# Performance work log

Measured on AMD Instinct MI355X. Metric: run time of the kernel, lower is better.

Reference implementation:

```python
import jax, jax.numpy as jnp
import numpy as np
from jax import lax

B, N, C, H, W = 2, 32, 64, 128, 128
ROI_H = ROI_W = 28
RATIO = 2  # ROIAlign sampling_ratio


def setup_inputs() -> dict:
    key = jax.random.key(0)
    ks = jax.random.split(key, 20)
    p = lambda k, s: jax.random.normal(k, s, jnp.float32) * 0.05
    inp = {}
    inp['cnn_feature'] = jax.random.normal(ks[0], (B, C, H, W), jnp.float32)
    inp['act_ind'] = jax.random.randint(ks[1], (B, N), 0, H * W)
    inp['awh'] = jax.random.uniform(ks[2], (B, N, 2), jnp.float32, minval=4.0, maxval=40.0)
    # fusion: 4 convs (64->256, then 256->256 x3), all 3x3 pad 1
    inp['w1'] = p(ks[3], (256, 64, 3, 3)); inp['b1'] = jnp.zeros((256,), jnp.float32)
    inp['w2'] = p(ks[4], (256, 256, 3, 3)); inp['b2'] = jnp.zeros((256,), jnp.float32)
    inp['w3'] = p(ks[5], (256, 256, 3, 3)); inp['b3'] = jnp.zeros((256,), jnp.float32)
    inp['w4'] = p(ks[6], (256, 256, 3, 3)); inp['b4'] = jnp.zeros((256,), jnp.float32)
    # cp_hm head: deconv(256->256,k2,s2) + conv1x1(256->1), bias -2.19
    inp['hm_dw'] = p(ks[7], (256, 256, 2, 2))  # torch ConvTranspose layout [in,out,kh,kw]
    inp['hm_db'] = jnp.zeros((256,), jnp.float32)
    inp['hm_w'] = p(ks[8], (1, 256, 1, 1)); inp['hm_b'] = jnp.full((1,), -2.19, jnp.float32)
    # cp_wh head: deconv(256->256,k2,s2) + conv1x1(256->2), bias 0
    inp['wh_dw'] = p(ks[9], (256, 256, 2, 2))
    inp['wh_db'] = jnp.zeros((256,), jnp.float32)
    inp['wh_w'] = p(ks[10], (2, 256, 1, 1)); inp['wh_b'] = jnp.zeros((2,), jnp.float32)
    return inp


def conv(x, w, b, pad):
    y = lax.conv_general_dilated(x, w, (1, 1), pad, dimension_numbers=('NCHW', 'OIHW', 'NCHW'))
    return y + b[None, :, None, None]


def deconv2x2s2(x, w, b):
    # matches torch ConvTranspose2d(k=2, s=2, pad=0) with weight [in,out,2,2]
    y = lax.conv_transpose(x, w, (2, 2), 'VALID', dimension_numbers=('NCHW', 'IOHW', 'NCHW'), transpose_kernel=True)
    return y + b[None, :, None, None]


def roi_align(feat, b_idx, boxes):
    # feat [B,C,H,W], boxes [R,4] (x1,y1,x2,y2), spatial_scale=1, sampling_ratio=RATIO
    x1, y1, x2, y2 = boxes[:, 0], boxes[:, 1], boxes[:, 2], boxes[:, 3]
    bw = (x2 - x1) / ROI_W
    bh = (y2 - y1) / ROI_H
    sx = jnp.arange(ROI_W * RATIO)
    sy = jnp.arange(ROI_H * RATIO)
    # sample coord for bin i, sub-sample k: start + (i + (k+0.5)/ratio) * bin
    fx = (sx // RATIO).astype(jnp.float32) + ((sx % RATIO).astype(jnp.float32) + 0.5) / RATIO
    fy = (sy // RATIO).astype(jnp.float32) + ((sy % RATIO).astype(jnp.float32) + 0.5) / RATIO
    xs = x1[:, None] + fx[None, :] * bw[:, None]   # [R,Sx]
    ys = y1[:, None] + fy[None, :] * bh[:, None]   # [R,Sy]

    def sample_one(bi, ysr, xsr):
        img = feat[bi]                              # [C,H,W]
        ysr = jnp.clip(ysr, 0.0, H - 1.0)
        xsr = jnp.clip(xsr, 0.0, W - 1.0)
        y0 = jnp.floor(ysr).astype(jnp.int32); y1i = jnp.minimum(y0 + 1, H - 1); wy = ysr - y0
        x0 = jnp.floor(xsr).astype(jnp.int32); x1i = jnp.minimum(x0 + 1, W - 1); wx = xsr - x0
        # separable bilinear: interpolate rows, then columns
        rows = img[:, y0, :] * (1.0 - wy)[None, :, None] + img[:, y1i, :] * wy[None, :, None]  # [C,Sy,W]
        vals = rows[:, :, x0] * (1.0 - wx)[None, None, :] + rows[:, :, x1i] * wx[None, None, :]  # [C,Sy,Sx]
        # average RATIO x RATIO samples per bin
        v = vals.reshape(C, ROI_H, RATIO, ROI_W, RATIO)
        return v.mean(axis=(2, 4))                  # [C,ROI_H,ROI_W]

    return jax.vmap(sample_one)(b_idx, ys, xs)      # [R,C,ROI_H,ROI_W]


def reference(cnn_feature, act_ind, awh, w1, b1, w2, b2, w3, b3, w4, b4,
              hm_dw, hm_db, hm_w, hm_b, wh_dw, wh_db, wh_w, wh_b):
    # --- prepare_training: decode boxes from act_ind + awh (act_01 all ones) ---
    xs = (act_ind % W).astype(jnp.float32)          # [B,N]
    ys = (act_ind // W).astype(jnp.float32)
    half_w = awh[..., 0] / 2.0
    half_h = awh[..., 1] / 2.0
    boxes = jnp.stack([xs - half_w, ys - half_h, xs + half_w, ys + half_h], axis=-1)  # [B,N,4]
    boxes = boxes.reshape(B * N, 4)
    b_idx = jnp.repeat(jnp.arange(B), N)
    roi = roi_align(cnn_feature, b_idx, boxes)      # [R,64,28,28]
    # --- fusion convs ---
    x = jax.nn.relu(conv(roi, w1, b1, 'SAME'))
    x = jax.nn.relu(conv(x, w2, b2, 'SAME'))
    x = jax.nn.relu(conv(x, w3, b3, 'SAME'))
    x = jax.nn.relu(conv(x, w4, b4, 'SAME'))        # [R,256,28,28]
    # --- heads ---
    cp_hm = conv(deconv2x2s2(x, hm_dw, hm_db), hm_w, hm_b, 'VALID')  # [R,1,56,56]
    cp_wh = conv(deconv2x2s2(x, wh_dw, wh_db), wh_w, wh_b, 'VALID')  # [R,2,56,56]
    return jnp.concatenate([cp_hm, cp_wh], axis=1)  # [R,3,56,56]
```

## Files before the change

kernel.cpp:

```cpp
#include <hip/hip_runtime.h>
#include <hip/hip_bf16.h>

#define HWF 128
#define NB  64
#define PW  30
#define PP  900

using bf16 = __hip_bfloat16;
typedef __attribute__((ext_vector_type(8)))  short short8;
typedef __attribute__((ext_vector_type(4)))  float f32x4;
typedef __attribute__((ext_vector_type(16))) float f32x16;
typedef __attribute__((ext_vector_type(4)))  unsigned int u32x4;
typedef __attribute__((ext_vector_type(2)))  unsigned int u32x2;

__device__ __forceinline__ float b2f(bf16 v) { return __bfloat162float(v); }
__device__ __forceinline__ bf16  f2b(float v){ return __float2bfloat16(v); }
__device__ __forceinline__ float u2f(unsigned short u){ unsigned x = (unsigned)u << 16; float f; __builtin_memcpy(&f,&x,4); return f; }
__device__ __forceinline__ unsigned pack2(float a, float b) {
  union { bf16 h; unsigned short u; } ca, cb; ca.h = f2b(a); cb.h = f2b(b);
  return ((unsigned)cb.u << 16) | (unsigned)ca.u;
}

__global__ void weff_kernel(const float* __restrict__ hm_dw, const float* __restrict__ hm_db,
                            const float* __restrict__ hm_w,  const float* __restrict__ hm_b,
                            const float* __restrict__ wh_dw, const float* __restrict__ wh_db,
                            const float* __restrict__ wh_w,  const float* __restrict__ wh_b,
                            float* __restrict__ Weff, float* __restrict__ beff) {
  const int blk = blockIdx.x;
  const int k = blk / 3, o = blk % 3;
  const int ci = threadIdx.x;
  const float* dw = (o == 0) ? hm_dw : wh_dw;
  const float* hw = (o == 0) ? hm_w  : (wh_w + (size_t)(o - 1) * 256);
  const float* dwp = dw + (size_t)ci * 4 + k;
  float s = 0.f;
  for (int co = 0; co < 256; ++co) s += hw[co] * dwp[(size_t)co * 1024];
  Weff[(size_t)blk * 256 + ci] = s;
  if (k == 0 && ci == 0) {
    const float* db = (o == 0) ? hm_db : wh_db;
    float bb = (o == 0) ? hm_b[0] : wh_b[o - 1];
    float t = 0.f;
    for (int co = 0; co < 256; ++co) t += hw[co] * db[co];
    beff[o] = bb + t;
  }
}

__global__ void wt_kernel(const float* __restrict__ w, bf16* __restrict__ Wt, int CIN) {
  const int co = blockIdx.x, ci = threadIdx.x;
  const int NCIB = CIN >> 5;
  const int cib = ci >> 5, cl = ci & 31;
  const int kh = cl >> 4, koct = (cl >> 3) & 1, e = ci & 7;
  for (int tap = 0; tap < 9; ++tap)
    Wt[(((((size_t)tap * NCIB + cib) * 2 + kh) * 256 + co) * 2 + koct) * 8 + e]
        = f2b(w[((size_t)co * CIN + ci) * 9 + tap]);
}

__global__ __launch_bounds__(256) void featT_kernel(const float* __restrict__ feat,
                                                    bf16* __restrict__ featT) {
  const int by = blockIdx.x;
  const int b = by >> 7, y = by & 127;
  const int t = threadIdx.x;
  __shared__ float tile[128][65];
  const int xr = t & 127, c2 = t >> 7;
  for (int c0 = 0; c0 < 64; c0 += 2)
    tile[xr][c0 + c2] = feat[(((size_t)(b * 64 + c0 + c2) * 128 + y) * 128) + xr];
  __syncthreads();
  const int cw = t & 63, x4 = t >> 6;
  for (int x0 = 0; x0 < 128; x0 += 4)
    featT[(((size_t)by * 128) + x0 + x4) * 64 + cw] = f2b(tile[x0 + x4][cw]);
}

__global__ __launch_bounds__(256) void roi_cl(const bf16* __restrict__ featT,
                                              const int* __restrict__ act_ind,
                                              const float* __restrict__ awh,
                                              bf16* __restrict__ roiP) {
  const int r = blockIdx.x, part = blockIdx.y;
  const int t = threadIdx.x;
  if (part == 7) {
    for (int i = t; i < 116 * 64; i += 256) {
      int j = i >> 6, c = i & 63;
      int py, px;
      if (j < 30)      { py = 0;      px = j;      }
      else if (j < 60) { py = 29;     px = j - 30; }
      else if (j < 88) { py = j - 59; px = 0;      }
      else             { py = j - 87; px = 29;     }
      roiP[(((size_t)(r * 2 + (c >> 5)) * PP) + py * PW + px) * 32 + (c & 31)] = f2b(0.f);
    }
    return;
  }
  const int wave = t >> 6, c = t & 63;
  const int bi = r >> 5;
  const int ind = act_ind[r];
  const float cx = (float)(ind % HWF), cy = (float)(ind / HWF);
  const float hw = awh[r * 2 + 0] * 0.5f, hh = awh[r * 2 + 1] * 0.5f;
  const float x1b = cx - hw, y1b = cy - hh;
  const float bw = hw / 14.f, bh = hh / 14.f;
  const bf16* fb = featT + (size_t)bi * HWF * HWF * 64;
  for (int pp = part * 112 + wave; pp < part * 112 + 112; pp += 4) {
    int ry = pp / 28, rx = pp % 28;
    float acc = 0.f;
#pragma unroll
    for (int a = 0; a < 2; ++a) {
      int syi = 2 * ry + a;
      float ys = y1b + ((float)syi * 0.5f + 0.25f) * bh;
      ys = fminf(fmaxf(ys, 0.f), 127.f);
      int y0 = (int)floorf(ys); int y1i = min(y0 + 1, 127);
      float wy = ys - (float)y0;
#pragma unroll
      for (int b2 = 0; b2 < 2; ++b2) {
        int sxi = 2 * rx + b2;
        float xs = x1b + ((float)sxi * 0.5f + 0.25f) * bw;
        xs = fminf(fmaxf(xs, 0.f), 127.f);
        int x0 = (int)floorf(xs); int x1i = min(x0 + 1, 127);
        float wx = xs - (float)x0;
        float v00 = b2f(fb[((size_t)y0  * HWF + x0 ) * 64 + c]);
        float v01 = b2f(fb[((size_t)y0  * HWF + x1i) * 64 + c]);
        float v10 = b2f(fb[((size_t)y1i * HWF + x0 ) * 64 + c]);
        float v11 = b2f(fb[((size_t)y1i * HWF + x1i) * 64 + c]);
        float r0 = v00 * (1.f - wy) + v10 * wy;
        float r1 = v01 * (1.f - wy) + v11 * wy;
        acc += r0 * (1.f - wx) + r1 * wx;
      }
    }
    int slot = (ry + 1) * PW + (rx + 1);
    roiP[(((size_t)(r * 2 + (c >> 5)) * PP) + slot) * 32 + (c & 31)] = f2b(acc * 0.25f);
  }
}

template <int CIN>
__global__ __launch_bounds__(256, 2) void conv_mfma(const bf16* __restrict__ X,
                                                    const bf16* __restrict__ Wt,
                                                    const float* __restrict__ bias,
                                                    bf16* __restrict__ Y) {
  constexpr int NCIB = CIN / 32;
  const int d = blockIdx.x;
  const int xcd = d & 7, sub = d >> 3;
  const int img = xcd * 8 + (sub >> 4);
  const int sm  = sub & 15;
  const int sb  = sm >> 2;
  const int mg  = sm & 3;
  const int s0  = 30 + sb * 210;
  const int gbase = s0 - 31;
  const int t = threadIdx.x;
  const int wave = t >> 6, lane = t & 63;
  const int hi = lane >> 5, l31 = lane & 31;
  const int ng = wave;

  __shared__ char lds_raw[71680];
  char* Ab = lds_raw;
  char* Bb = lds_raw + 36864;

  int bsrc[5]; bool bok[5];
#pragma unroll
  for (int r = 0; r < 5; ++r) {
    int chunk = r * 256 + t;
    bok[r] = (chunk < 1088);
    int ss = chunk >> 2, up = chunk & 3;
    int u = up ^ ((ss >> 2) & 3);
    int q = gbase + ss; q = q < 0 ? 0 : (q > 899 ? 899 : q);
    bsrc[r] = q * 64 + u * 16;
  }

#define STAGE_B(BSEL, CIB)                                                       \
  {                                                                              \
    const char* Xc = (const char*)X + ((size_t)(img * NCIB + (CIB)) * 900) * 64; \
    _Pragma("unroll")                                                            \
    for (int r = 0; r < 5; ++r) {                                                \
      if (bok[r]) {                                                              \
        __builtin_amdgcn_global_load_lds(                                        \
            (const __attribute__((address_space(1))) unsigned int*)(Xc + bsrc[r]),\
            (__attribute__((address_space(3))) unsigned int*)                    \
                (Bb + (BSEL) * 17408 + r * 4096 + wave * 1024), 16, 0, 0);       \
      }                                                                          \
    }                                                                            \
  }

  const int kh_w = t >> 7;
  const int cl127 = t & 127;

#define STAGE_A(CIB)                                                             \
  {                                                                              \
    _Pragma("unroll")                                                            \
    for (int t9 = 0; t9 < 9; ++t9) {                                             \
      const char* src = (const char*)Wt +                                        \
          (((size_t)(t9 * NCIB + (CIB)) * 2 + kh_w) * 8192) + mg * 2048          \
          + cl127 * 16;                                                          \
      __builtin_amdgcn_global_load_lds(                                          \
          (const __attribute__((address_space(1))) unsigned int*)src,            \
          (__attribute__((address_space(3))) unsigned int*)                      \
              (Ab + t9 * 4096 + wave * 1024), 16, 0, 0);                         \
    }                                                                            \
  }

  f32x16 acc[2][2];
#pragma unroll
  for (int mf = 0; mf < 2; ++mf)
#pragma unroll
    for (int nf = 0; nf < 2; ++nf)
#pragma unroll
      for (int e = 0; e < 16; ++e) acc[mf][nf][e] = 0.f;

  int soc[2];
#pragma unroll
  for (int nf = 0; nf < 2; ++nf) {
    int so = ng * 64 + nf * 32 + l31;
    soc[nf] = (so > 209 ? 209 : so) + 31;
  }

  constexpr int DTP[9] = { -31, -30, -29, -1, 0, 1, 29, 30, 31 };

#define LOADA(A, J)                                                              \
  {                                                                              \
    _Pragma("unroll")                                                            \
    for (int mf = 0; mf < 2; ++mf) {                                             \
      A[mf] = *(const short8*)(Ab + ((J) >> 1) * 4096 + ((J) & 1) * 2048         \
                               + (mf * 32 + l31) * 32 + hi * 16);                \
    }                                                                            \
  }

#define LOADB(B, LB, J)                                                          \
  {                                                                              \
    _Pragma("unroll")                                                            \
    for (int nf = 0; nf < 2; ++nf) {                                             \
      int ss = soc[nf] + DTP[(J) >> 1];                                          \
      int u = ((((J) & 1) << 1) + hi) ^ ((ss >> 2) & 3);                         \
      B[nf] = *(const short8*)((LB) + ss * 64 + (u << 4));                       \
    }                                                                            \
  }

#define DOMFMA(A, B)                                                             \
  {                                                                              \
    _Pragma("unroll")                                                            \
    for (int mf = 0; mf < 2; ++mf)                                               \
      _Pragma("unroll")                                                          \
      for (int nf = 0; nf < 2; ++nf)                                             \
        acc[mf][nf] = __builtin_amdgcn_mfma_f32_32x32x16_bf16(                   \
            A[mf], B[nf], acc[mf][nf], 0, 0, 0);                                 \
  }

  STAGE_A(0);
  STAGE_B(0, 0);
  __syncthreads();

  int cur = 0;
  for (int k = 0; k < NCIB; ++k) {
    if (k + 1 < NCIB) STAGE_B(cur ^ 1, k + 1);
    const char* lb = Bb + cur * 17408;

    short8 a0[2], b0[2], a1[2], b1[2];
    LOADA(a0, 0); LOADB(b0, lb, 0);
#pragma unroll
    for (int j = 0; j < 18; j += 2) {
      if (j + 1 < 18) { LOADA(a1, j + 1); LOADB(b1, lb, j + 1); }
      DOMFMA(a0, b0);
      if (j + 2 < 18) { LOADA(a0, j + 2); LOADB(b0, lb, j + 2); }
      if (j + 1 < 18) DOMFMA(a1, b1);
    }
    __syncthreads();
    if (k + 1 < NCIB) {
      STAGE_A(k + 1);
      __syncthreads();
    }
    cur ^= 1;
  }

  {
    f32x4 bv[2][4];
#pragma unroll
    for (int mf = 0; mf < 2; ++mf)
#pragma unroll
      for (int rq = 0; rq < 4; ++rq)
        bv[mf][rq] = *(const f32x4*)(bias + mg * 64 + mf * 32 + 8 * rq + 4 * hi);
#pragma unroll
    for (int mf = 0; mf < 2; ++mf) {
#pragma unroll
      for (int nf = 0; nf < 2; ++nf) {
        int so = ng * 64 + nf * 32 + l31;
        if (so < 210) {
#pragma unroll
          for (int rq = 0; rq < 4; ++rq) {
            float r0 = fmaxf(acc[mf][nf][4*rq+0] + bv[mf][rq][0], 0.f);
            float r1 = fmaxf(acc[mf][nf][4*rq+1] + bv[mf][rq][1], 0.f);
            float r2 = fmaxf(acc[mf][nf][4*rq+2] + bv[mf][rq][2], 0.f);
            float r3 = fmaxf(acc[mf][nf][4*rq+3] + bv[mf][rq][3], 0.f);
            u32x2 pk; pk.x = pack2(r0, r1); pk.y = pack2(r2, r3);
            int cb = mf * 64 + rq * 16 + hi * 8;
            *(u32x2*)(lds_raw + so * 128 + ((cb + so * 8) & 127)) = pk;
          }
        }
      }
    }
  }
  __syncthreads();

  {
#pragma unroll
    for (int p = 0; p < 7; ++p) {
      int idx = p * 256 + t;
      if (idx < 1680) {
        int slot = idx >> 3, rem = idx & 7;
        int cob_l = rem >> 2, q = rem & 3;
        int gslot = s0 + slot;
        int c = gslot % 30;
        u32x4 o;
        if (c == 0 || c == 29) { o.x = 0u; o.y = 0u; o.z = 0u; o.w = 0u; }
        else {
          int cb0 = cob_l * 64 + q * 16;
          u32x2 v0 = *(u32x2*)(lds_raw + slot * 128 + ((cb0 + 0 + slot * 8) & 127));
          u32x2 v1 = *(u32x2*)(lds_raw + slot * 128 + ((cb0 + 8 + slot * 8) & 127));
          o.x = v0.x; o.y = v0.y; o.z = v1.x; o.w = v1.y;
        }
        *(u32x4*)((char*)Y + ((size_t)(img * 8 + mg * 2 + cob_l) * 900 + gslot) * 64
                  + q * 16) = o;
      }
    }
  }
  if (sb == 0 || sb == 3) {
    const int rowslot = (sb == 0) ? 0 : 870;
    if (t < 240) {
      int slot_z = t >> 3, rem = t & 7;
      int cob_l = rem >> 2, q = rem & 3;
      if (q < 4 && cob_l < 2) {
        u32x4 z; z.x = 0u; z.y = 0u; z.z = 0u; z.w = 0u;
        *(u32x4*)((char*)Y + ((size_t)(img * 8 + mg * 2 + cob_l) * 900
                  + rowslot + slot_z) * 64 + q * 16) = z;
      }
    }
  }
}

__global__ __launch_bounds__(256) void head_cl(const bf16* __restrict__ X,
                                               const float* __restrict__ Weff,
                                               const float* __restrict__ beff,
                                               float* __restrict__ out) {
  const int idx = blockIdx.x * 256 + threadIdx.x;
  const int img = idx / 784, p = idx % 784;
  const float bo0 = beff[0], bo1 = beff[1], bo2 = beff[2];
  int iy = p / 28, ix = p % 28;
  int slot = (iy + 1) * PW + ix + 1;
  float acc[12];
#pragma unroll
  for (int k = 0; k < 12; ++k) acc[k] = 0.f;
  for (int cob = 0; cob < 8; ++cob) {
    const bf16* xp = X + ((size_t)(img * 8 + cob) * PP + slot) * 32;
#pragma unroll
    for (int oct = 0; oct < 4; ++oct) {
      short8 v = *(const short8*)(xp + oct * 8);
#pragma unroll
      for (int j = 0; j < 8; ++j) {
        float xv = u2f((unsigned short)v[j]);
        int ci = cob * 32 + oct * 8 + j;
#pragma unroll
        for (int k = 0; k < 12; ++k)
          acc[k] += xv * Weff[k * 256 + ci];
      }
    }
  }
#pragma unroll
  for (int k4 = 0; k4 < 4; ++k4) {
    int oy = 2 * iy + (k4 >> 1), ox = 2 * ix + (k4 & 1);
    out[(((size_t)(img * 3 + 0)) * 56 + oy) * 56 + ox] = acc[k4 * 3 + 0] + bo0;
    out[(((size_t)(img * 3 + 1)) * 56 + oy) * 56 + ox] = acc[k4 * 3 + 1] + bo1;
    out[(((size_t)(img * 3 + 2)) * 56 + oy) * 56 + ox] = acc[k4 * 3 + 2] + bo2;
  }
}

extern "C" void kernel_launch(void* const* d_in, const int* in_sizes, int n_in,
                              void* d_out, int out_size, void* d_ws, size_t ws_size,
                              hipStream_t stream) {
  const float* feat    = (const float*)d_in[0];
  const int*   act_ind = (const int*)  d_in[1];
  const float* awh     = (const float*)d_in[2];
  const float* w1 = (const float*)d_in[3];  const float* b1 = (const float*)d_in[4];
  const float* w2 = (const float*)d_in[5];  const float* b2 = (const float*)d_in[6];
  const float* w3 = (const float*)d_in[7];  const float* b3 = (const float*)d_in[8];
  const float* w4 = (const float*)d_in[9];  const float* b4 = (const float*)d_in[10];
  const float* hm_dw = (const float*)d_in[11]; const float* hm_db = (const float*)d_in[12];
  const float* hm_w  = (const float*)d_in[13]; const float* hm_b  = (const float*)d_in[14];
  const float* wh_dw = (const float*)d_in[15]; const float* wh_db = (const float*)d_in[16];
  const float* wh_w  = (const float*)d_in[17]; const float* wh_b  = (const float*)d_in[18];

  char* ws = (char*)d_ws;
  size_t offset = 0;
  auto alloc = [&](size_t bytes) {
    size_t r = offset;
    offset += (bytes + 255) & ~(size_t)255;
    return r;
  };
  float* Weff = (float*)(ws + alloc(12 * 256 * sizeof(float)));
  float* beff = (float*)(ws + alloc(256));
  bf16*  Wt1  = (bf16*)(ws + alloc((size_t)9 * 256 * 64  * 2));
  bf16*  Wt2  = (bf16*)(ws + alloc((size_t)9 * 256 * 256 * 2));
  bf16*  Wt3  = (bf16*)(ws + alloc((size_t)9 * 256 * 256 * 2));
  bf16*  Wt4  = (bf16*)(ws + alloc((size_t)9 * 256 * 256 * 2));
  bf16*  bufA = (bf16*)(ws + alloc((size_t)NB * 256 * PP * 2));
  bf16*  bufB = (bf16*)(ws + alloc((size_t)NB * 256 * PP * 2));
  bf16*  roiP  = bufB;
  bf16*  featT = (bf16*)((char*)bufB + (8u << 20));

  weff_kernel<<<12, 256, 0, stream>>>(hm_dw, hm_db, hm_w, hm_b,
                                      wh_dw, wh_db, wh_w, wh_b, Weff, beff);
  wt_kernel<<<256, 64,  0, stream>>>(w1, Wt1, 64);
  wt_kernel<<<256, 256, 0, stream>>>(w2, Wt2, 256);
  wt_kernel<<<256, 256, 0, stream>>>(w3, Wt3, 256);
  wt_kernel<<<256, 256, 0, stream>>>(w4, Wt4, 256);
  featT_kernel<<<256, 256, 0, stream>>>(feat, featT);
  roi_cl<<<dim3(NB, 8), 256, 0, stream>>>(featT, act_ind, awh, roiP);
  conv_mfma<64> <<<1024, 256, 0, stream>>>(roiP, Wt1, b1, bufA);
  conv_mfma<256><<<1024, 256, 0, stream>>>(bufA, Wt2, b2, bufB);
  conv_mfma<256><<<1024, 256, 0, stream>>>(bufB, Wt3, b3, bufA);
  conv_mfma<256><<<1024, 256, 0, stream>>>(bufA, Wt4, b4, bufB);
  head_cl<<<196, 256, 0, stream>>>(bufB, Weff, beff, (float*)d_out);
}
```

Baseline: 344.1 us.

## Split weight staging by k-half with double-buffered A and swizzled LDS layout

Weight (A) tiles were staged once per input-channel block, followed by a blocking barrier. They are now split into two k-halves held in separate LDS buffers, so loading the next half overlaps with MFMA work on the current half. The A layout in LDS gains an XOR swizzle to reduce bank conflicts on the fragment reads. This costs more LDS space and one extra barrier per iteration, and it depends on the new A-buffer offsets not colliding with the B buffers.

```diff
diff --git a/kernel.cpp b/kernel.cpp
--- a/kernel.cpp
+++ b/kernel.cpp
@@ -174,20 +174,27 @@
     }                                                                            \
   }
 
-  const int kh_w = t >> 7;
-  const int cl127 = t & 127;
-
-#define STAGE_A(CIB)                                                             \
-  {                                                                              \
+  int asr[5]; bool aok[5];
+#pragma unroll
+  for (int r = 0; r < 5; ++r) {
+    int chunk = r * 256 + t;
+    aok[r] = (chunk < 1152);
+    int tap = chunk >> 7, within = chunk & 127;
+    int s = within ^ ((within >> 3) & 7);
+    asr[r] = tap * (NCIB * 2 * 8192) + mg * 2048 + s * 16;
+  }
+
+#define STAGE_A(CIB, KH, ABSEL)                                                  \
+  {                                                                              \
+    const char* Wb = (const char*)Wt + ((CIB) * 2 + (KH)) * 8192;                \
     _Pragma("unroll")                                                            \
-    for (int t9 = 0; t9 < 9; ++t9) {                                             \
-      const char* src = (const char*)Wt +                                        \
-          (((size_t)(t9 * NCIB + (CIB)) * 2 + kh_w) * 8192) + mg * 2048          \
-          + cl127 * 16;                                                          \
-      __builtin_amdgcn_global_load_lds(                                          \
-          (const __attribute__((address_space(1))) unsigned int*)src,            \
-          (__attribute__((address_space(3))) unsigned int*)                      \
-              (Ab + t9 * 4096 + wave * 1024), 16, 0, 0);                         \
+    for (int r = 0; r < 5; ++r) {                                                \
+      if (aok[r]) {                                                              \
+        __builtin_amdgcn_global_load_lds(                                        \
+            (const __attribute__((address_space(1))) unsigned int*)(Wb + asr[r]),\
+            (__attribute__((address_space(3))) unsigned int*)                    \
+                (Ab + (ABSEL) * 18432 + (r * 256 + wave * 64) * 16), 16, 0, 0);  \
+      }                                                                          \
     }                                                                            \
   }
 
@@ -205,24 +212,24 @@
     int so = ng * 64 + nf * 32 + l31;
     soc[nf] = (so > 209 ? 209 : so) + 31;
   }
-
-  constexpr int DTP[9] = { -31, -30, -29, -1, 0, 1, 29, 30, 31 };
-
-#define LOADA(A, J)                                                              \
+  const int gl0 = 2 * l31 + hi;
+  const int apos = (gl0 ^ ((gl0 >> 3) & 7)) * 16;
+
+  constexpr int DTP9[9] = { -31, -30, -29, -1, 0, 1, 29, 30, 31 };
+
+#define LOADA(A, AB, T)                                                          \
   {                                                                              \
     _Pragma("unroll")                                                            \
-    for (int mf = 0; mf < 2; ++mf) {                                             \
-      A[mf] = *(const short8*)(Ab + ((J) >> 1) * 4096 + ((J) & 1) * 2048         \
-                               + (mf * 32 + l31) * 32 + hi * 16);                \
-    }                                                                            \
-  }
-
-#define LOADB(B, LB, J)                                                          \
+    for (int mf = 0; mf < 2; ++mf)                                               \
+      A[mf] = *(const short8*)((AB) + (T) * 2048 + mf * 1024 + apos);            \
+  }
+
+#define LOADB(B, LB, T, KH)                                                      \
   {                                                                              \
     _Pragma("unroll")                                                            \
     for (int nf = 0; nf < 2; ++nf) {                                             \
-      int ss = soc[nf] + DTP[(J) >> 1];                                          \
-      int u = ((((J) & 1) << 1) + hi) ^ ((ss >> 2) & 3);                         \
+      int ss = soc[nf] + DTP9[(T)];                                              \
+      int u = (((KH) << 1) + hi) ^ ((ss >> 2) & 3);                              \
       B[nf] = *(const short8*)((LB) + ss * 64 + (u << 4));                       \
     }                                                                            \
   }
@@ -237,29 +244,42 @@
             A[mf], B[nf], acc[mf][nf], 0, 0, 0);                                 \
   }
 
-  STAGE_A(0);
+#define JLOOP(KH, AB, LB)                                                        \
+  {                                                                              \
+    short8 a0[2], b0[2], a1[2], b1[2];                                           \
+    LOADA(a0, AB, 0); LOADB(b0, LB, 0, KH);                                      \
+    LOADA(a1, AB, 1); LOADB(b1, LB, 1, KH);                                      \
+    DOMFMA(a0, b0);                                                              \
+    LOADA(a0, AB, 2); LOADB(b0, LB, 2, KH);                                      \
+    DOMFMA(a1, b1);                                                              \
+    LOADA(a1, AB, 3); LOADB(b1, LB, 3, KH);                                      \
+    DOMFMA(a0, b0);                                                              \
+    LOADA(a0, AB, 4); LOADB(b0, LB, 4, KH);                                      \
+    DOMFMA(a1, b1);                                                              \
+    LOADA(a1, AB, 5); LOADB(b1, LB, 5, KH);                                      \
+    DOMFMA(a0, b0);                                                              \
+    LOADA(a0, AB, 6); LOADB(b0, LB, 6, KH);                                      \
+    DOMFMA(a1, b1);                                                              \
+    LOADA(a1, AB, 7); LOADB(b1, LB, 7, KH);                                      \
+    DOMFMA(a0, b0);                                                              \
+    LOADA(a0, AB, 8); LOADB(b0, LB, 8, KH);                                      \
+    DOMFMA(a1, b1);                                                              \
+    DOMFMA(a0, b0);                                                              \
+  }
+
+  STAGE_A(0, 0, 0);
   STAGE_B(0, 0);
   __syncthreads();
 
   int cur = 0;
-  for (int k = 0; k < NCIB; ++k) {
-    if (k + 1 < NCIB) STAGE_B(cur ^ 1, k + 1);
-    const char* lb = Bb + cur * 17408;
-
-    short8 a0[2], b0[2], a1[2], b1[2];
-    LOADA(a0, 0); LOADB(b0, lb, 0);
-#pragma unroll
-    for (int j = 0; j < 18; j += 2) {
-      if (j + 1 < 18) { LOADA(a1, j + 1); LOADB(b1, lb, j + 1); }
-      DOMFMA(a0, b0);
-      if (j + 2 < 18) { LOADA(a0, j + 2); LOADB(b0, lb, j + 2); }
-      if (j + 1 < 18) DOMFMA(a1, b1);
-    }
+  for (int cib = 0; cib < NCIB; ++cib) {
+    STAGE_A(cib, 1, 1);
+    if (cib + 1 < NCIB) STAGE_B(cur ^ 1, cib + 1);
+    JLOOP(0, Ab, Bb + cur * 17408);
     __syncthreads();
-    if (k + 1 < NCIB) {
-      STAGE_A(k + 1);
-      __syncthreads();
-    }
+    if (cib + 1 < NCIB) STAGE_A(cib + 1, 0, 0);
+    JLOOP(1, Ab + 18432, Bb + cur * 17408);
+    __syncthreads();
     cur ^= 1;
   }
 
```

Result: no change. 342.8 us (-0.4%).
